# Kernel tuning notes

Hardware: AMD Instinct MI355X
Metric: run time of the kernel (lower is better)

Reference implementation:

```python
import jax, jax.numpy as jnp
import numpy as np

B, K, N, F_IN, F_OUT, T = 8, 3, 2048, 16, 64, 12


def setup_inputs() -> dict:
    key = jax.random.key(0)
    k1, k2, k3, k4 = jax.random.split(key, 4)
    x = jax.random.normal(k1, (B, N, F_IN, T), dtype=jnp.float32)
    spatial_attention = jax.random.normal(k2, (B, K, N, N), dtype=jnp.float32)
    adj = jax.random.uniform(k3, (N, N), dtype=jnp.float32)  # fusiongraph() output
    Theta = jax.random.normal(k4, (K, F_IN, F_OUT), dtype=jnp.float32) * 0.1
    return {"x": x, "spatial_attention": spatial_attention, "adj": adj, "Theta": Theta}


def _cheb_polynomials(L_tilde, k_order):
    # NOTE: original uses ELEMENTWISE multiply in the recurrence (L_tilde * T_{k-1}),
    # faithfully reproduced here.
    n = L_tilde.shape[0]
    polys = [jnp.eye(n, dtype=L_tilde.dtype), L_tilde]
    for _ in range(2, k_order):
        polys.append(2.0 * L_tilde * polys[-1] - polys[-2])
    return jnp.stack(polys[:k_order], axis=0)  # (K, N, N)


def reference(x, spatial_attention, adj, Theta):
    # Unnormalized graph Laplacian L = D - A (torch_geometric get_laplacian default).
    deg = jnp.sum(adj, axis=1)                      # (N,)
    L_tilde = jnp.diag(deg) - adj                   # (N, N)
    cheb = _cheb_polynomials(L_tilde, K)            # (K, N, N)

    # softmax over dim=1 of each (B,N,N) slice -> axis=2 of (B,K,N,N); time-invariant.
    attn = jax.nn.softmax(spatial_attention, axis=2)  # (B, K, N, N)
    Tka = cheb[None, :, :, :] * attn                  # (B, K, N, N)

    # rhs[b,n,f,t] = sum_m Tka[b,k,m,n] * x[b,m,f,t]; out = rhs @ Theta_k, summed over k.
    out = jnp.einsum('bkmn,bmft,kfo->bnot', Tka, x, Theta)  # (B, N, F_OUT, T)
    return jax.nn.relu(out)
```

## Files before the change

### kernel.cpp

```cpp
#include <hip/hip_runtime.h>


#define NB 8
#define NN 2048
#define FT 192
#define BN 32
#define BM 64
#define LBM 72
#define ZST 33

typedef __attribute__((ext_vector_type(8))) short short8;
typedef __attribute__((ext_vector_type(4))) float f32x4;

__device__ __forceinline__ unsigned short bf16_rne(float f) {
  unsigned u = __float_as_uint(f);
  u += 0x7FFFu + ((u >> 16) & 1u);
  return (unsigned short)(u >> 16);
}

__device__ __forceinline__ void gload_lds16(const float* g, float* l) {
  __builtin_amdgcn_global_load_lds(
      (const __attribute__((address_space(1))) void*)g,
      (__attribute__((address_space(3))) void*)l, 16, 0, 0);
}

__global__ __launch_bounds__(256) void k_prep(const float* __restrict__ adj,
                                              float* __restrict__ deg,
                                              const float* __restrict__ x,
                                              unsigned short* __restrict__ xT) {
  __shared__ float ls[4];
  const int bid = blockIdx.x;
  if (bid < NN) {
    const float* r = adj + (size_t)bid * NN;
    float s = 0.f;
    for (int j = threadIdx.x; j < NN; j += 256) s += r[j];
    for (int off = 32; off; off >>= 1) s += __shfl_down(s, off, 64);
    if ((threadIdx.x & 63) == 0) ls[threadIdx.x >> 6] = s;
    __syncthreads();
    if (threadIdx.x == 0) deg[bid] = ls[0] + ls[1] + ls[2] + ls[3];
  } else {
    const int xbk = bid - NN;
    const int b = xbk >> 6, m0 = (xbk & 63) * 32;
    const int ft = threadIdx.x;
    if (ft < FT) {
      const float* src = x + (size_t)b * NN * FT + ft;
      uint4* dst = (uint4*)(xT + ((size_t)b * FT + ft) * NN + m0);
#pragma unroll
      for (int g = 0; g < 4; ++g) {
        unsigned u[4];
#pragma unroll
        for (int j = 0; j < 4; ++j) {
          float lo = src[(size_t)(m0 + g * 8 + 2 * j) * FT];
          float hi = src[(size_t)(m0 + g * 8 + 2 * j + 1) * FT];
          u[j] = (unsigned)bf16_rne(lo) | ((unsigned)bf16_rne(hi) << 16);
        }
        dst[g] = make_uint4(u[0], u[1], u[2], u[3]);
      }
    }
  }
}

__global__ __launch_bounds__(256, 2) void k_fused(
    const float* __restrict__ Sall, const float* __restrict__ adj,
    const float* __restrict__ deg, const unsigned short* __restrict__ xT,
    const float* __restrict__ x, const float* __restrict__ Theta,
    float* __restrict__ out) {
  __shared__ __align__(16) char smem[74752];
  __shared__ float dEs[BN];
  __shared__ float sc[3][BN];

  float* const SrA1 = (float*)smem;
  float* const SrA2 = (float*)(smem + 8192);
  float* const SrB1 = (float*)(smem + 16384);
  float* const SrB2 = (float*)(smem + 24576);
  unsigned short* const PtB = (unsigned short*)(smem + 32768);

  const int flat = blockIdx.x + (blockIdx.y << 6);
  const int b = flat & 7;
  const int tile = flat >> 3;
  const int n0 = tile * BN;

  const int t = threadIdx.x;
  const int lane = t & 63, w = t >> 6;
  const int ln = lane & 15, quad = lane >> 4;
  const int col4 = (t & 7) << 2;
  const int rowg = t >> 3;
  const int srow = lane >> 3;
  const int scol = (lane & 7) << 2;

  const float* S0 = Sall + (size_t)b * 3 * NN * NN;
  const float* S1 = S0 + (size_t)NN * NN;
  const float* S2 = S1 + (size_t)NN * NN;
  const unsigned short* xbp = xT + (size_t)b * FT * NN;

  const int cdiag = n0 >> 6;
  const float4 dgv = *(const float4*)(deg + n0 + col4);

  const f32x4 zero4 = {0.f, 0.f, 0.f, 0.f};
  f32x4 acc1[2][3], acc2[2][3];
#pragma unroll
  for (int i = 0; i < 2; ++i)
#pragma unroll
    for (int q = 0; q < 3; ++q) {
      acc1[i][q] = zero4;
      acc2[i][q] = zero4;
    }
  float zp0[4] = {0.f, 0.f, 0.f, 0.f};
  float zp1[4] = {0.f, 0.f, 0.f, 0.f};
  float zp2[4] = {0.f, 0.f, 0.f, 0.f};

  auto STAGE = [&](int c, float* d1, float* d2) {
    const int m0s = c * BM;
#pragma unroll
    for (int j2 = 0; j2 < 2; ++j2) {
      const int r0 = (w << 4) + (j2 << 3);
      const size_t go = (size_t)(m0s + r0 + srow) * NN + n0 + scol;
      gload_lds16(S1 + go, d1 + r0 * BN);
      gload_lds16(S2 + go, d2 + r0 * BN);
    }
  };

  auto LOADAV = [&](int c, float4 av[2], float4 sv[2]) {
#pragma unroll
    for (int r = 0; r < 2; ++r) {
      const int gm = c * BM + rowg * 2 + r;
      av[r] = *(const float4*)(adj + (size_t)gm * NN + n0 + col4);
      sv[r] = *(const float4*)(S0 + (size_t)gm * NN + n0 + col4);
    }
  };

  auto PACK = [&](int c, int pbuf, const float* R1, const float* R2,
                  const float4 av[2], const float4 sv[2]) {
    const bool isd = (c == cdiag);
    unsigned short* P1 = PtB + (size_t)pbuf * 2304;
    unsigned short* P2 = PtB + (size_t)(2 + pbuf) * 2304;
    unsigned short q1[2][4], q2[2][4];
    const float dg[4] = {dgv.x, dgv.y, dgv.z, dgv.w};
#pragma unroll
    for (int r = 0; r < 2; ++r) {
      const int lrow = rowg * 2 + r;
      const float4 s1 = *(const float4*)&R1[lrow * BN + col4];
      const float4 s2 = *(const float4*)&R2[lrow * BN + col4];
      const float se1[4] = {s1.x, s1.y, s1.z, s1.w};
      const float se2[4] = {s2.x, s2.y, s2.z, s2.w};
      const float aa[4] = {av[r].x, av[r].y, av[r].z, av[r].w};
      const float s0e[4] = {sv[r].x, sv[r].y, sv[r].z, sv[r].w};
#pragma unroll
      for (int j = 0; j < 4; ++j) {
        const float e0 = __expf(s0e[j]);
        const float e1 = __expf(se1[j]);
        const float e2 = __expf(se2[j]);
        zp0[j] += e0;
        zp1[j] += e1;
        zp2[j] += e2;
        float c1 = -aa[j];
        float c2 = 2.f * aa[j] * aa[j];
        if (isd) {
          if (c * BM + lrow == n0 + col4 + j) {
            const float L = dg[j] - aa[j];
            c1 = L;
            c2 = 2.f * L * L - 1.f;
            dEs[col4 + j] = e0;
          }
        }
        q1[r][j] = bf16_rne(e1 * c1);
        q2[r][j] = bf16_rne(e2 * c2);
      }
    }
#pragma unroll
    for (int j = 0; j < 4; ++j) {
      const unsigned v1 = (unsigned)q1[0][j] | ((unsigned)q1[1][j] << 16);
      const unsigned v2 = (unsigned)q2[0][j] | ((unsigned)q2[1][j] << 16);
      *(unsigned*)&P1[(col4 + j) * LBM + rowg * 2] = v1;
      *(unsigned*)&P2[(col4 + j) * LBM + rowg * 2] = v2;
    }
  };

  auto BFR = [&](int c, short8 bfr[2][3]) {
    const int m0 = c * BM;
#pragma unroll
    for (int ks2 = 0; ks2 < 2; ++ks2)
#pragma unroll
      for (int q = 0; q < 3; ++q)
        bfr[ks2][q] = *(const short8*)(xbp +
            (size_t)(w * 48 + q * 16 + ln) * NN + m0 + ks2 * 32 + quad * 8);
  };

  auto MFMAh = [&](int pbuf, const short8 bfr[2][3]) {
#pragma unroll
    for (int ks2 = 0; ks2 < 2; ++ks2) {
      short8 a1[2], a2[2];
#pragma unroll
      for (int i = 0; i < 2; ++i) {
        a1[i] = *(const short8*)&PtB[(size_t)pbuf * 2304 + (i * 16 + ln) * LBM +
                                     ks2 * 32 + quad * 8];
        a2[i] = *(const short8*)&PtB[(size_t)(2 + pbuf) * 2304 +
                                     (i * 16 + ln) * LBM + ks2 * 32 + quad * 8];
      }
#pragma unroll
      for (int i = 0; i < 2; ++i)
#pragma unroll
        for (int q = 0; q < 3; ++q) {
          acc1[i][q] = __builtin_amdgcn_mfma_f32_16x16x32_bf16(
              a1[i], bfr[ks2][q], acc1[i][q], 0, 0, 0);
          acc2[i][q] = __builtin_amdgcn_mfma_f32_16x16x32_bf16(
              a2[i], bfr[ks2][q], acc2[i][q], 0, 0, 0);
        }
    }
  };

  float4 avA[2], svA[2], avB[2], svB[2];

  STAGE(0, SrA1, SrA2);
  LOADAV(0, avA, svA);
  asm volatile("s_waitcnt vmcnt(0)" ::: "memory");
  __builtin_amdgcn_sched_barrier(0);
  PACK(0, 0, SrA1, SrA2, avA, svA);
  STAGE(1, SrB1, SrB2);
  LOADAV(1, avB, svB);
  asm volatile("s_waitcnt lgkmcnt(0)" ::: "memory");
  __builtin_amdgcn_s_barrier();

  for (int c2 = 0; c2 < 32; c2 += 2) {
    {
      short8 bfr[2][3];
      BFR(c2, bfr);
      __builtin_amdgcn_sched_barrier(0);
      if (c2 + 2 < 32) {
        STAGE(c2 + 2, SrA1, SrA2);
        LOADAV(c2 + 2, avA, svA);
      }
      __builtin_amdgcn_sched_barrier(0);
      MFMAh(0, bfr);
      asm volatile("s_waitcnt vmcnt(8)" ::: "memory");
      __builtin_amdgcn_sched_barrier(0);
      PACK(c2 + 1, 1, SrB1, SrB2, avB, svB);
      asm volatile("s_waitcnt lgkmcnt(0)" ::: "memory");
      __builtin_amdgcn_s_barrier();
    }
    {
      short8 bfr[2][3];
      BFR(c2 + 1, bfr);
      __builtin_amdgcn_sched_barrier(0);
      if (c2 + 3 < 32) {
        STAGE(c2 + 3, SrB1, SrB2);
        LOADAV(c2 + 3, avB, svB);
      }
      __builtin_amdgcn_sched_barrier(0);
      MFMAh(1, bfr);
      asm volatile("s_waitcnt vmcnt(8)" ::: "memory");
      __builtin_amdgcn_sched_barrier(0);
      if (c2 + 2 < 32) PACK(c2 + 2, 0, SrA1, SrA2, avA, svA);
      asm volatile("s_waitcnt lgkmcnt(0)" ::: "memory");
      __builtin_amdgcn_s_barrier();
    }
  }

  float* Zr = (float*)smem;
#pragma unroll
  for (int j = 0; j < 4; ++j) {
    Zr[0 * 32 * ZST + rowg * ZST + col4 + j] = zp0[j];
    Zr[1 * 32 * ZST + rowg * ZST + col4 + j] = zp1[j];
    Zr[2 * 32 * ZST + rowg * ZST + col4 + j] = zp2[j];
  }
  __syncthreads();
  if (t < 96) {
    const int which = t >> 5, n = t & 31;
    float Z = 0.f;
#pragma unroll
    for (int g = 0; g < 32; ++g) Z += Zr[which * 32 * ZST + g * ZST + n];
    sc[which][n] = (which == 0) ? (dEs[n] / Z) : (1.f / Z);
  }
  __syncthreads();

  float* const r1s = (float*)smem;
  float* const r2s = (float*)(smem + 25088);
  float* const xs = (float*)(smem + 50176);
#pragma unroll
  for (int i = 0; i < 2; ++i)
#pragma unroll
    for (int q = 0; q < 3; ++q) {
      const int ft = w * 48 + q * 16 + ln;
#pragma unroll
      for (int r = 0; r < 4; ++r) {
        const int nl = i * 16 + quad * 4 + r;
        r1s[nl * 196 + ft] = acc1[i][q][r];
        r2s[nl * 196 + ft] = acc2[i][q][r];
      }
    }
  for (int l = t; l < 32 * 48; l += 256) {
    const int row = l / 48, c4 = (l % 48) * 4;
    *(float4*)&xs[row * 192 + c4] =
        *(const float4*)(x + ((size_t)b * NN + n0 + row) * FT + c4);
  }
  __syncthreads();

  const int o = t & 63, nl2 = t >> 6;
  float th0[16], th1[16], th2[16];
#pragma unroll
  for (int f = 0; f < 16; ++f) {
    th0[f] = Theta[f * 64 + o];
    th1[f] = Theta[(16 + f) * 64 + o];
    th2[f] = Theta[(32 + f) * 64 + o];
  }
#pragma unroll 1
  for (int ni = 0; ni < 8; ++ni) {
    const int n = ni * 4 + nl2;
    float a0[12], a1[12], a2[12];
#pragma unroll
    for (int e = 0; e < 12; ++e) a0[e] = a1[e] = a2[e] = 0.f;
#pragma unroll
    for (int f = 0; f < 16; ++f) {
      const f32x4* xv = (const f32x4*)&xs[n * 192 + f * 12];
      const f32x4* r1v = (const f32x4*)&r1s[n * 196 + f * 12];
      const f32x4* r2v = (const f32x4*)&r2s[n * 196 + f * 12];
#pragma unroll
      for (int g = 0; g < 3; ++g)
#pragma unroll
        for (int e = 0; e < 4; ++e) {
          a0[g * 4 + e] += th0[f] * xv[g][e];
          a1[g * 4 + e] += th1[f] * r1v[g][e];
          a2[g * 4 + e] += th2[f] * r2v[g][e];
        }
    }
    const float c0 = sc[0][n], rz1 = sc[1][n], rz2 = sc[2][n];
    float4* op = (float4*)(out + (((size_t)b * NN + n0 + n) * 64 + o) * 12);
#pragma unroll
    for (int g = 0; g < 3; ++g) {
      float4 rv;
      rv.x = fmaxf(a0[g * 4 + 0] * c0 + a1[g * 4 + 0] * rz1 + a2[g * 4 + 0] * rz2, 0.f);
      rv.y = fmaxf(a0[g * 4 + 1] * c0 + a1[g * 4 + 1] * rz1 + a2[g * 4 + 1] * rz2, 0.f);
      rv.z = fmaxf(a0[g * 4 + 2] * c0 + a1[g * 4 + 2] * rz1 + a2[g * 4 + 2] * rz2, 0.f);
      rv.w = fmaxf(a0[g * 4 + 3] * c0 + a1[g * 4 + 3] * rz1 + a2[g * 4 + 3] * rz2, 0.f);
      op[g] = rv;
    }
  }
}

extern "C" void kernel_launch(void* const* d_in, const int* in_sizes, int n_in,
                              void* d_out, int out_size, void* d_ws,
                              size_t ws_size, hipStream_t stream) {
  (void)in_sizes;
  (void)n_in;
  (void)out_size;
  const float* x = (const float*)d_in[0];
  const float* s_attn = (const float*)d_in[1];
  const float* adj = (const float*)d_in[2];
  const float* Theta = (const float*)d_in[3];
  float* out = (float*)d_out;
  char* ws = (char*)d_ws;

  const size_t szXT = (size_t)NB * FT * NN * 2;
  const size_t szDeg = NN * 4;
  if (ws_size < szXT + szDeg) return;

  unsigned short* xT = (unsigned short*)ws;
  float* deg = (float*)(ws + szXT);

  hipLaunchKernelGGL(k_prep, dim3(NN + 512), dim3(256), 0, stream, adj, deg, x,
                     xT);
  hipLaunchKernelGGL(k_fused, dim3(64, NB), dim3(256), 0, stream, s_attn, adj,
                     deg, xT, x, Theta, out);
}
```

Baseline: 654.0 us.

## Widen fused kernel node tile to 64 with 512-thread blocks

Doubles the output-node tile per block from 32 to 64 and uses 8 waves split into node-half and feature groups. Each xT B-fragment loaded from global memory now serves twice as many output columns, cutting redundant xT reads. Blocks drop from 512 to 256 and LDS per block grows to about 100KB, so occupancy falls and the epilogue is serialized into two halves with extra barriers. The grid then covers fewer blocks than there are CUs on the device, which risks underusing the GPU.

```diff
diff --git a/kernel.cpp b/kernel.cpp
--- a/kernel.cpp
+++ b/kernel.cpp
@@ -4,10 +4,9 @@
 #define NB 8
 #define NN 2048
 #define FT 192
-#define BN 32
+#define BN 64
 #define BM 64
 #define LBM 72
-#define ZST 33
 
 typedef __attribute__((ext_vector_type(8))) short short8;
 typedef __attribute__((ext_vector_type(4))) float f32x4;
@@ -60,40 +59,41 @@
   }
 }
 
-__global__ __launch_bounds__(256, 2) void k_fused(
+__global__ __launch_bounds__(512, 2) void k_fused(
     const float* __restrict__ Sall, const float* __restrict__ adj,
     const float* __restrict__ deg, const unsigned short* __restrict__ xT,
     const float* __restrict__ x, const float* __restrict__ Theta,
     float* __restrict__ out) {
-  __shared__ __align__(16) char smem[74752];
+  __shared__ __align__(16) char smem[102400];
   __shared__ float dEs[BN];
   __shared__ float sc[3][BN];
 
   float* const SrA1 = (float*)smem;
-  float* const SrA2 = (float*)(smem + 8192);
-  float* const SrB1 = (float*)(smem + 16384);
-  float* const SrB2 = (float*)(smem + 24576);
-  unsigned short* const PtB = (unsigned short*)(smem + 32768);
-
-  const int flat = blockIdx.x + (blockIdx.y << 6);
+  float* const SrA2 = (float*)(smem + 16384);
+  float* const SrB1 = (float*)(smem + 32768);
+  float* const SrB2 = (float*)(smem + 49152);
+  unsigned short* const PtB = (unsigned short*)(smem + 65536);
+
+  const int flat = blockIdx.x + (blockIdx.y << 5);
   const int b = flat & 7;
   const int tile = flat >> 3;
   const int n0 = tile * BN;
 
   const int t = threadIdx.x;
   const int lane = t & 63, w = t >> 6;
+  const int wn = w & 1, wf = w >> 1;
   const int ln = lane & 15, quad = lane >> 4;
-  const int col4 = (t & 7) << 2;
-  const int rowg = t >> 3;
-  const int srow = lane >> 3;
-  const int scol = (lane & 7) << 2;
+  const int col4 = (t & 15) << 2;
+  const int rowg = t >> 4;
+  const int srow = lane >> 4;
+  const int scol = (lane & 15) << 2;
 
   const float* S0 = Sall + (size_t)b * 3 * NN * NN;
   const float* S1 = S0 + (size_t)NN * NN;
   const float* S2 = S1 + (size_t)NN * NN;
   const unsigned short* xbp = xT + (size_t)b * FT * NN;
 
-  const int cdiag = n0 >> 6;
+  const int cdiag = tile;
   const float4 dgv = *(const float4*)(deg + n0 + col4);
 
   const f32x4 zero4 = {0.f, 0.f, 0.f, 0.f};
@@ -113,7 +113,7 @@
     const int m0s = c * BM;
 #pragma unroll
     for (int j2 = 0; j2 < 2; ++j2) {
-      const int r0 = (w << 4) + (j2 << 3);
+      const int r0 = (w << 3) + (j2 << 2);
       const size_t go = (size_t)(m0s + r0 + srow) * NN + n0 + scol;
       gload_lds16(S1 + go, d1 + r0 * BN);
       gload_lds16(S2 + go, d2 + r0 * BN);
@@ -132,8 +132,8 @@
   auto PACK = [&](int c, int pbuf, const float* R1, const float* R2,
                   const float4 av[2], const float4 sv[2]) {
     const bool isd = (c == cdiag);
-    unsigned short* P1 = PtB + (size_t)pbuf * 2304;
-    unsigned short* P2 = PtB + (size_t)(2 + pbuf) * 2304;
+    unsigned short* P1 = PtB + (size_t)pbuf * 4608;
+    unsigned short* P2 = PtB + (size_t)(2 + pbuf) * 4608;
     unsigned short q1[2][4], q2[2][4];
     const float dg[4] = {dgv.x, dgv.y, dgv.z, dgv.w};
 #pragma unroll
@@ -156,7 +156,7 @@
         float c1 = -aa[j];
         float c2 = 2.f * aa[j] * aa[j];
         if (isd) {
-          if (c * BM + lrow == n0 + col4 + j) {
+          if (lrow == col4 + j) {
             const float L = dg[j] - aa[j];
             c1 = L;
             c2 = 2.f * L * L - 1.f;
@@ -183,7 +183,7 @@
 #pragma unroll
       for (int q = 0; q < 3; ++q)
         bfr[ks2][q] = *(const short8*)(xbp +
-            (size_t)(w * 48 + q * 16 + ln) * NN + m0 + ks2 * 32 + quad * 8);
+            (size_t)(wf * 48 + q * 16 + ln) * NN + m0 + ks2 * 32 + quad * 8);
   };
 
   auto MFMAh = [&](int pbuf, const short8 bfr[2][3]) {
@@ -192,10 +192,11 @@
       short8 a1[2], a2[2];
 #pragma unroll
       for (int i = 0; i < 2; ++i) {
-        a1[i] = *(const short8*)&PtB[(size_t)pbuf * 2304 + (i * 16 + ln) * LBM +
+        const int prow = wn * 32 + i * 16 + ln;
+        a1[i] = *(const short8*)&PtB[(size_t)pbuf * 4608 + prow * LBM +
                                      ks2 * 32 + quad * 8];
-        a2[i] = *(const short8*)&PtB[(size_t)(2 + pbuf) * 2304 +
-                                     (i * 16 + ln) * LBM + ks2 * 32 + quad * 8];
+        a2[i] = *(const short8*)&PtB[(size_t)(2 + pbuf) * 4608 + prow * LBM +
+                                     ks2 * 32 + quad * 8];
       }
 #pragma unroll
       for (int i = 0; i < 2; ++i)
@@ -259,16 +260,16 @@
   float* Zr = (float*)smem;
 #pragma unroll
   for (int j = 0; j < 4; ++j) {
-    Zr[0 * 32 * ZST + rowg * ZST + col4 + j] = zp0[j];
-    Zr[1 * 32 * ZST + rowg * ZST + col4 + j] = zp1[j];
-    Zr[2 * 32 * ZST + rowg * ZST + col4 + j] = zp2[j];
+    Zr[(0 * 32 + rowg) * 64 + col4 + j] = zp0[j];
+    Zr[(1 * 32 + rowg) * 64 + col4 + j] = zp1[j];
+    Zr[(2 * 32 + rowg) * 64 + col4 + j] = zp2[j];
   }
   __syncthreads();
-  if (t < 96) {
-    const int which = t >> 5, n = t & 31;
+  if (t < 192) {
+    const int which = t >> 6, n = t & 63;
     float Z = 0.f;
 #pragma unroll
-    for (int g = 0; g < 32; ++g) Z += Zr[which * 32 * ZST + g * ZST + n];
+    for (int g = 0; g < 32; ++g) Z += Zr[(which * 32 + g) * 64 + n];
     sc[which][n] = (which == 0) ? (dEs[n] / Z) : (1.f / Z);
   }
   __syncthreads();
@@ -276,26 +277,7 @@
   float* const r1s = (float*)smem;
   float* const r2s = (float*)(smem + 25088);
   float* const xs = (float*)(smem + 50176);
-#pragma unroll
-  for (int i = 0; i < 2; ++i)
-#pragma unroll
-    for (int q = 0; q < 3; ++q) {
-      const int ft = w * 48 + q * 16 + ln;
-#pragma unroll
-      for (int r = 0; r < 4; ++r) {
-        const int nl = i * 16 + quad * 4 + r;
-        r1s[nl * 196 + ft] = acc1[i][q][r];
-        r2s[nl * 196 + ft] = acc2[i][q][r];
-      }
-    }
-  for (int l = t; l < 32 * 48; l += 256) {
-    const int row = l / 48, c4 = (l % 48) * 4;
-    *(float4*)&xs[row * 192 + c4] =
-        *(const float4*)(x + ((size_t)b * NN + n0 + row) * FT + c4);
-  }
-  __syncthreads();
-
-  const int o = t & 63, nl2 = t >> 6;
+  const int o = t & 63, nl8 = t >> 6;
   float th0[16], th1[16], th2[16];
 #pragma unroll
   for (int f = 0; f < 16; ++f) {
@@ -303,37 +285,63 @@
     th1[f] = Theta[(16 + f) * 64 + o];
     th2[f] = Theta[(32 + f) * 64 + o];
   }
+
 #pragma unroll 1
-  for (int ni = 0; ni < 8; ++ni) {
-    const int n = ni * 4 + nl2;
-    float a0[12], a1[12], a2[12];
-#pragma unroll
-    for (int e = 0; e < 12; ++e) a0[e] = a1[e] = a2[e] = 0.f;
-#pragma unroll
-    for (int f = 0; f < 16; ++f) {
-      const f32x4* xv = (const f32x4*)&xs[n * 192 + f * 12];
-      const f32x4* r1v = (const f32x4*)&r1s[n * 196 + f * 12];
-      const f32x4* r2v = (const f32x4*)&r2s[n * 196 + f * 12];
-#pragma unroll
-      for (int g = 0; g < 3; ++g)
-#pragma unroll
-        for (int e = 0; e < 4; ++e) {
-          a0[g * 4 + e] += th0[f] * xv[g][e];
-          a1[g * 4 + e] += th1[f] * r1v[g][e];
-          a2[g * 4 + e] += th2[f] * r2v[g][e];
+  for (int p = 0; p < 2; ++p) {
+    if (wn == p) {
+#pragma unroll
+      for (int i = 0; i < 2; ++i)
+#pragma unroll
+        for (int q = 0; q < 3; ++q) {
+          const int ft = wf * 48 + q * 16 + ln;
+#pragma unroll
+          for (int r = 0; r < 4; ++r) {
+            const int nl = i * 16 + quad * 4 + r;
+            r1s[nl * 196 + ft] = acc1[i][q][r];
+            r2s[nl * 196 + ft] = acc2[i][q][r];
+          }
         }
     }
-    const float c0 = sc[0][n], rz1 = sc[1][n], rz2 = sc[2][n];
-    float4* op = (float4*)(out + (((size_t)b * NN + n0 + n) * 64 + o) * 12);
-#pragma unroll
-    for (int g = 0; g < 3; ++g) {
-      float4 rv;
-      rv.x = fmaxf(a0[g * 4 + 0] * c0 + a1[g * 4 + 0] * rz1 + a2[g * 4 + 0] * rz2, 0.f);
-      rv.y = fmaxf(a0[g * 4 + 1] * c0 + a1[g * 4 + 1] * rz1 + a2[g * 4 + 1] * rz2, 0.f);
-      rv.z = fmaxf(a0[g * 4 + 2] * c0 + a1[g * 4 + 2] * rz1 + a2[g * 4 + 2] * rz2, 0.f);
-      rv.w = fmaxf(a0[g * 4 + 3] * c0 + a1[g * 4 + 3] * rz1 + a2[g * 4 + 3] * rz2, 0.f);
-      op[g] = rv;
-    }
+    for (int l = t; l < 32 * 48; l += 512) {
+      const int row = l / 48, c4 = (l % 48) * 4;
+      *(float4*)&xs[row * 192 + c4] =
+          *(const float4*)(x + ((size_t)b * NN + n0 + p * 32 + row) * FT + c4);
+    }
+    __syncthreads();
+#pragma unroll 1
+    for (int ni = 0; ni < 4; ++ni) {
+      const int n = ni * 8 + nl8;
+      float a0[12], a1[12], a2[12];
+#pragma unroll
+      for (int e = 0; e < 12; ++e) a0[e] = a1[e] = a2[e] = 0.f;
+#pragma unroll
+      for (int f = 0; f < 16; ++f) {
+        const f32x4* xv = (const f32x4*)&xs[n * 192 + f * 12];
+        const f32x4* r1v = (const f32x4*)&r1s[n * 196 + f * 12];
+        const f32x4* r2v = (const f32x4*)&r2s[n * 196 + f * 12];
+#pragma unroll
+        for (int g = 0; g < 3; ++g)
+#pragma unroll
+          for (int e = 0; e < 4; ++e) {
+            a0[g * 4 + e] += th0[f] * xv[g][e];
+            a1[g * 4 + e] += th1[f] * r1v[g][e];
+            a2[g * 4 + e] += th2[f] * r2v[g][e];
+          }
+      }
+      const int gn = p * 32 + n;
+      const float c0 = sc[0][gn], rz1 = sc[1][gn], rz2 = sc[2][gn];
+      float4* op = (float4*)(out + (((size_t)b * NN + n0 + gn) * 64 + o) * 12);
+#pragma unroll
+      for (int g = 0; g < 3; ++g) {
+        float4 rv;
+        rv.x = fmaxf(a0[g * 4 + 0] * c0 + a1[g * 4 + 0] * rz1 + a2[g * 4 + 0] * rz2, 0.f);
+        rv.y = fmaxf(a0[g * 4 + 1] * c0 + a1[g * 4 + 1] * rz1 + a2[g * 4 + 1] * rz2, 0.f);
+        rv.z = fmaxf(a0[g * 4 + 2] * c0 + a1[g * 4 + 2] * rz1 + a2[g * 4 + 2] * rz2, 0.f);
+        rv.w = fmaxf(a0[g * 4 + 3] * c0 + a1[g * 4 + 3] * rz1 + a2[g * 4 + 3] * rz2, 0.f);
+        op[g] = rv;
+      }
+    }
+    __syncthreads();
   }
 }
 
@@ -359,6 +367,6 @@
 
   hipLaunchKernelGGL(k_prep, dim3(NN + 512), dim3(256), 0, stream, adj, deg, x,
                      xT);
-  hipLaunchKernelGGL(k_fused, dim3(64, NB), dim3(256), 0, stream, s_attn, adj,
+  hipLaunchKernelGGL(k_fused, dim3(32, NB), dim3(512), 0, stream, s_attn, adj,
                      deg, xT, x, Theta, out);
 }
```

New measurement: 617.0 us. 5.7% less time.
